# Kernel optimization log

Measured on AMD Instinct MI355X. Metric: run time of the kernel, lower is better.

The kernel has to match this reference:

```python
import jax, jax.numpy as jnp
import numpy as np

B, T, C, NH = 4, 2048, 1024, 16
HS = C // NH


def setup_inputs() -> dict:
    key = jax.random.key(0)
    k1, k2, k3, k4, k5 = jax.random.split(key, 5)
    s = 1.0 / np.sqrt(C)
    return {
        "x": jax.random.normal(k1, (B, T, C), dtype=jnp.float32),
        "Wqkv": jax.random.normal(k2, (3 * C, C), dtype=jnp.float32) * s,
        "bqkv": jax.random.normal(k3, (3 * C,), dtype=jnp.float32) * 0.02,
        "Wproj": jax.random.normal(k4, (C, C), dtype=jnp.float32) * s,
        "bproj": jax.random.normal(k5, (C,), dtype=jnp.float32) * 0.02,
    }


def reference(x, Wqkv, bqkv, Wproj, bproj):
    Bsz, Tlen, Cdim = x.shape
    # qkv projection (torch Linear: x @ W.T + b)
    qkv = x @ Wqkv.T + bqkv                      # [B, T, 3C]
    q, k, v = jnp.split(qkv, 3, axis=-1)
    # [B, NH, T, HS]
    q = q.reshape(Bsz, Tlen, NH, HS).transpose(0, 2, 1, 3)
    k = k.reshape(Bsz, Tlen, NH, HS).transpose(0, 2, 1, 3)
    v = v.reshape(Bsz, Tlen, NH, HS).transpose(0, 2, 1, 3)
    scale = 1.0 / np.sqrt(HS)
    att = jnp.einsum('bhqd,bhkd->bhqk', q, k) * scale
    causal = jnp.triu(jnp.ones((Tlen, Tlen), dtype=bool), k=1)
    att = jnp.where(causal[None, None], -jnp.inf, att)
    att = jax.nn.softmax(att, axis=-1)
    y = jnp.einsum('bhqk,bhkd->bhqd', att, v)    # [B, NH, T, HS]
    y = y.transpose(0, 2, 1, 3).reshape(Bsz, Tlen, Cdim)
    return y @ Wproj.T + bproj
```

## Files before the change

kernel.cpp:

```cpp
#include <hip/hip_runtime.h>
#include <hip/hip_bf16.h>

#define B_   4
#define T_   2048
#define C_   1024
#define NH_  16
#define HS_  64
#define M_   8192
#define N1_  3072
#define BH_  64

typedef __attribute__((ext_vector_type(8))) short short8;
typedef __attribute__((ext_vector_type(4))) short short4v;
typedef __attribute__((ext_vector_type(4))) float f32x4;

#define QSCALE 0.18033688011112042f

__device__ __forceinline__ short f2bf(float f) {
  unsigned u = __float_as_uint(f);
  unsigned r = (u + 0x7fffu + ((u >> 16) & 1u)) >> 16;
  return (short)r;
}
__device__ __forceinline__ unsigned pk_bf16(float a, float b) {
  __hip_bfloat162 h = __float22bfloat162_rn(make_float2(a, b));
  union { __hip_bfloat162 h2; unsigned u; } cv; cv.h2 = h; return cv.u;
}

typedef __attribute__((address_space(1))) unsigned int as1_uint;
typedef __attribute__((address_space(3))) unsigned int as3_uint;
__device__ __forceinline__ void g2l16(const void* g, void* l) {
  __builtin_amdgcn_global_load_lds((as1_uint*)g, (as3_uint*)l, 16, 0, 0);
}

__global__ __launch_bounds__(256) void conv_bf16(
    const float* __restrict__ src, short* __restrict__ dst)
{
  const size_t i = ((size_t)blockIdx.x * 256 + threadIdx.x) * 8;
  const f32x4 a = *(const f32x4*)&src[i];
  const f32x4 b = *(const f32x4*)&src[i + 4];
  short8 o;
  o[0] = f2bf(a[0]); o[1] = f2bf(a[1]); o[2] = f2bf(a[2]); o[3] = f2bf(a[3]);
  o[4] = f2bf(b[0]); o[5] = f2bf(b[1]); o[6] = f2bf(b[2]); o[7] = f2bf(b[3]);
  *(short8*)&dst[i] = o;
}

__global__ __launch_bounds__(256) void qkv_gemm(
    const short* __restrict__ X,
    const short* __restrict__ W,
    const float* __restrict__ bias,
    short* __restrict__ Qo, short* __restrict__ Ko, short* __restrict__ Vt)
{
  __shared__ short As[2][128 * 64];
  __shared__ short Bs[2][128 * 64];
  const int tid = threadIdx.x;
  const int lane = tid & 63;
  const int wid = tid >> 6;
  const int wy = wid >> 1, wx = wid & 1;
  const int lq = lane >> 4, lm = lane & 15;
  const int row0 = blockIdx.x * 128;
  const int col0 = blockIdx.y * 128;

  f32x4 acc[4][4] = {};

  const int ar = tid >> 3;
  const int ac = (tid & 7) << 3;

#pragma unroll
  for (int j = 0; j < 4; ++j) {
    const int r = ar + j * 32;
    g2l16(&X[(size_t)(row0 + r) * C_ + ac], &As[0][r * 64 + ac]);
    g2l16(&W[(size_t)(col0 + r) * C_ + ac], &Bs[0][r * 64 + ac]);
  }
  __syncthreads();

  int cur = 0;
  for (int k0 = 0; k0 < C_; k0 += 64) {
    if (k0 + 64 < C_) {
#pragma unroll
      for (int j = 0; j < 4; ++j) {
        const int r = ar + j * 32;
        g2l16(&X[(size_t)(row0 + r) * C_ + k0 + 64 + ac], &As[cur ^ 1][r * 64 + ac]);
        g2l16(&W[(size_t)(col0 + r) * C_ + k0 + 64 + ac], &Bs[cur ^ 1][r * 64 + ac]);
      }
    }

#pragma unroll
    for (int kk = 0; kk < 2; ++kk) {
      short8 af[4], bfr[4];
#pragma unroll
      for (int mi = 0; mi < 4; ++mi)
        af[mi] = *(const short8*)&As[cur][(wy * 64 + mi * 16 + lm) * 64 + kk * 32 + lq * 8];
#pragma unroll
      for (int ni = 0; ni < 4; ++ni)
        bfr[ni] = *(const short8*)&Bs[cur][(wx * 64 + ni * 16 + lm) * 64 + kk * 32 + lq * 8];
#pragma unroll
      for (int mi = 0; mi < 4; ++mi)
#pragma unroll
        for (int ni = 0; ni < 4; ++ni)
          acc[mi][ni] = __builtin_amdgcn_mfma_f32_16x16x32_bf16(af[mi], bfr[ni], acc[mi][ni], 0, 0, 0);
    }

    __syncthreads();
    cur ^= 1;
  }

#pragma unroll
  for (int ni = 0; ni < 4; ++ni) {
    const int n = col0 + wx * 64 + ni * 16 + lm;
    const float bv = bias[n];
    const int sel = n >> 10;
    const int cc = n & (C_ - 1);
    const int h = cc >> 6, d = cc & 63;
    if (sel == 2) {
#pragma unroll
      for (int mi = 0; mi < 4; ++mi) {
        const int m0 = row0 + wy * 64 + mi * 16 + lq * 4;
        const int b = m0 >> 11, t0 = m0 & (T_ - 1);
        const int bh = b * NH_ + h;
        short4v o;
#pragma unroll
        for (int i = 0; i < 4; ++i) o[i] = f2bf(acc[mi][ni][i] + bv);
        *(short4v*)&Vt[((size_t)bh * HS_ + d) * T_ + t0] = o;
      }
    } else {
      short* dst = (sel == 0) ? Qo : Ko;
      const float qs = (sel == 0) ? QSCALE : 1.0f;
#pragma unroll
      for (int mi = 0; mi < 4; ++mi) {
#pragma unroll
        for (int i = 0; i < 4; ++i) {
          const int m = row0 + wy * 64 + mi * 16 + lq * 4 + i;
          const int b = m >> 11, t = m & (T_ - 1);
          const int bh = b * NH_ + h;
          dst[((size_t)bh * T_ + t) * HS_ + d] = f2bf((acc[mi][ni][i] + bv) * qs);
        }
      }
    }
  }
}

__global__ __launch_bounds__(256) void proj_gemm(
    const short* __restrict__ Y,
    const short* __restrict__ W,
    const float* __restrict__ bias,
    float* __restrict__ Out)
{
  __shared__ short As[2][128 * 64];
  __shared__ short Bs[2][128 * 64];
  const int tid = threadIdx.x;
  const int lane = tid & 63;
  const int wid = tid >> 6;
  const int wy = wid >> 1, wx = wid & 1;
  const int lq = lane >> 4, lm = lane & 15;
  const int row0 = blockIdx.x * 128;
  const int col0 = blockIdx.y * 128;

  f32x4 acc[4][4] = {};

  const int ar = tid >> 3;
  const int ac = (tid & 7) << 3;

#pragma unroll
  for (int j = 0; j < 4; ++j) {
    const int r = ar + j * 32;
    g2l16(&Y[(size_t)(row0 + r) * C_ + ac], &As[0][r * 64 + ac]);
    g2l16(&W[(size_t)(col0 + r) * C_ + ac], &Bs[0][r * 64 + ac]);
  }
  __syncthreads();

  int cur = 0;
  for (int k0 = 0; k0 < C_; k0 += 64) {
    if (k0 + 64 < C_) {
#pragma unroll
      for (int j = 0; j < 4; ++j) {
        const int r = ar + j * 32;
        g2l16(&Y[(size_t)(row0 + r) * C_ + k0 + 64 + ac], &As[cur ^ 1][r * 64 + ac]);
        g2l16(&W[(size_t)(col0 + r) * C_ + k0 + 64 + ac], &Bs[cur ^ 1][r * 64 + ac]);
      }
    }

#pragma unroll
    for (int kk = 0; kk < 2; ++kk) {
      short8 af[4], bfr[4];
#pragma unroll
      for (int mi = 0; mi < 4; ++mi)
        af[mi] = *(const short8*)&As[cur][(wy * 64 + mi * 16 + lm) * 64 + kk * 32 + lq * 8];
#pragma unroll
      for (int ni = 0; ni < 4; ++ni)
        bfr[ni] = *(const short8*)&Bs[cur][(wx * 64 + ni * 16 + lm) * 64 + kk * 32 + lq * 8];
#pragma unroll
      for (int mi = 0; mi < 4; ++mi)
#pragma unroll
        for (int ni = 0; ni < 4; ++ni)
          acc[mi][ni] = __builtin_amdgcn_mfma_f32_16x16x32_bf16(af[mi], bfr[ni], acc[mi][ni], 0, 0, 0);
    }

    __syncthreads();
    cur ^= 1;
  }

#pragma unroll
  for (int ni = 0; ni < 4; ++ni) {
    const int n = col0 + wx * 64 + ni * 16 + lm;
    const float bv = bias[n];
#pragma unroll
    for (int mi = 0; mi < 4; ++mi) {
#pragma unroll
      for (int i = 0; i < 4; ++i) {
        const int m = row0 + wy * 64 + mi * 16 + lq * 4 + i;
        Out[(size_t)m * C_ + n] = acc[mi][ni][i] + bv;
      }
    }
  }
}

#define LDK 72
__global__ __launch_bounds__(512, 4) void attn(
    const short* __restrict__ Qg, const short* __restrict__ Kg,
    const short* __restrict__ Vg, short* __restrict__ Yo)
{
  __shared__ short Ks[64 * LDK];
  __shared__ short Vs[64 * LDK];

  const int tid = threadIdx.x;
  const int lane = tid & 63;
  const int w = tid >> 6;
  const int wq = w & 3;
  const int grp = w >> 2;
  const int lq = lane >> 4, lm = lane & 15;
  const int bh = blockIdx.x;
  const int b = bh >> 4, h = bh & 15;
  const size_t base = (size_t)bh * T_ * HS_;
  const short* __restrict__ Kb = Kg + base;
  const short* __restrict__ Vb = Vg + base;

  const int sr = tid >> 3;
  const int sc = (tid & 7) * 8;

  const int ty = blockIdx.y;
  const int qt = grp ? ty : (15 - ty);
  const int nkt_g = 2 * qt + 2;
  const int nktA = 32 - 2 * ty;

  const int qA = qt * 128 + wq * 16 + lm;
  const int qB = qA + 64;

  const short8 qfA0 = *(const short8*)&Qg[base + (size_t)qA * HS_ + lq * 8];
  const short8 qfA1 = *(const short8*)&Qg[base + (size_t)qA * HS_ + 32 + lq * 8];
  const short8 qfB0 = *(const short8*)&Qg[base + (size_t)qB * HS_ + lq * 8];
  const short8 qfB1 = *(const short8*)&Qg[base + (size_t)qB * HS_ + 32 + lq * 8];

  float lA = 0.0f, lB = 0.0f;
  f32x4 oA[4] = {}, oB[4] = {};

  short8 pk = *(const short8*)&Kb[(size_t)sr * HS_ + sc];
  short8 pv = *(const short8*)&Vb[(size_t)sr * T_ + sc];

#pragma unroll 1
  for (int kt = 0; kt < nktA; ++kt) {
    const int kv0 = kt * 64;

    __syncthreads();
    *(short8*)&Ks[sr * LDK + sc] = pk;
    *(short8*)&Vs[sr * LDK + sc] = pv;
    __syncthreads();

    if (kt + 1 < nktA) {
      pk = *(const short8*)&Kb[(size_t)(kv0 + 64 + sr) * HS_ + sc];
      pv = *(const short8*)&Vb[(size_t)sr * T_ + kv0 + 64 + sc];
    }

    if (kt < nkt_g) {
      const bool doA = (kt <= 2 * qt);

      short8 kf0[4], kf1[4];
#pragma unroll
      for (int ni = 0; ni < 4; ++ni) {
        kf0[ni] = *(const short8*)&Ks[(ni * 16 + lm) * LDK + lq * 8];
        kf1[ni] = *(const short8*)&Ks[(ni * 16 + lm) * LDK + 32 + lq * 8];
      }

      f32x4 svA[4], svB[4];
      if (doA) {
#pragma unroll
        for (int ni = 0; ni < 4; ++ni) {
          f32x4 s = {};
          s = __builtin_amdgcn_mfma_f32_16x16x32_bf16(kf0[ni], qfA0, s, 0, 0, 0);
          svA[ni] = __builtin_amdgcn_mfma_f32_16x16x32_bf16(kf1[ni], qfA1, s, 0, 0, 0);
        }
      }
#pragma unroll
      for (int ni = 0; ni < 4; ++ni) {
        f32x4 s = {};
        s = __builtin_amdgcn_mfma_f32_16x16x32_bf16(kf0[ni], qfB0, s, 0, 0, 0);
        svB[ni] = __builtin_amdgcn_mfma_f32_16x16x32_bf16(kf1[ni], qfB1, s, 0, 0, 0);
      }

      if (kt == 2 * qt) {
#pragma unroll
        for (int ni = 0; ni < 4; ++ni) {
          const int kvb = kv0 + ni * 16 + lq * 4;
#pragma unroll
          for (int i = 0; i < 4; ++i)
            if (kvb + i > qA) svA[ni][i] = -3.0e38f;
        }
      }
      if (kt == 2 * qt + 1) {
#pragma unroll
        for (int ni = 0; ni < 4; ++ni) {
          const int kvb = kv0 + ni * 16 + lq * 4;
#pragma unroll
          for (int i = 0; i < 4; ++i)
            if (kvb + i > qB) svB[ni][i] = -3.0e38f;
        }
      }

      short4v p4A[4], p4B[4];
      if (doA) {
#pragma unroll
        for (int ni = 0; ni < 4; ++ni)
#pragma unroll
          for (int i = 0; i < 4; ++i)
            svA[ni][i] = __builtin_amdgcn_exp2f(svA[ni][i]);
        lA += ((svA[0][0] + svA[0][1]) + (svA[0][2] + svA[0][3]))
            + ((svA[1][0] + svA[1][1]) + (svA[1][2] + svA[1][3]))
            + ((svA[2][0] + svA[2][1]) + (svA[2][2] + svA[2][3]))
            + ((svA[3][0] + svA[3][1]) + (svA[3][2] + svA[3][3]));
#pragma unroll
        for (int ni = 0; ni < 4; ++ni) {
          union { short4v s4; unsigned u[2]; } pk2;
          pk2.u[0] = pk_bf16(svA[ni][0], svA[ni][1]);
          pk2.u[1] = pk_bf16(svA[ni][2], svA[ni][3]);
          p4A[ni] = pk2.s4;
        }
      }
#pragma unroll
      for (int ni = 0; ni < 4; ++ni)
#pragma unroll
        for (int i = 0; i < 4; ++i)
          svB[ni][i] = __builtin_amdgcn_exp2f(svB[ni][i]);
      lB += ((svB[0][0] + svB[0][1]) + (svB[0][2] + svB[0][3]))
          + ((svB[1][0] + svB[1][1]) + (svB[1][2] + svB[1][3]))
          + ((svB[2][0] + svB[2][1]) + (svB[2][2] + svB[2][3]))
          + ((svB[3][0] + svB[3][1]) + (svB[3][2] + svB[3][3]));
#pragma unroll
      for (int ni = 0; ni < 4; ++ni) {
        union { short4v s4; unsigned u[2]; } pk2;
        pk2.u[0] = pk_bf16(svB[ni][0], svB[ni][1]);
        pk2.u[1] = pk_bf16(svB[ni][2], svB[ni][3]);
        p4B[ni] = pk2.s4;
      }

      if (doA) {
#pragma unroll
        for (int di = 0; di < 4; ++di) {
#pragma unroll
          for (int ni = 0; ni < 4; ++ni) {
            const short4v vfr = *(const short4v*)&Vs[(di * 16 + lm) * LDK + ni * 16 + lq * 4];
            oA[di] = __builtin_amdgcn_mfma_f32_16x16x16bf16_1k(vfr, p4A[ni], oA[di], 0, 0, 0);
            oB[di] = __builtin_amdgcn_mfma_f32_16x16x16bf16_1k(vfr, p4B[ni], oB[di], 0, 0, 0);
          }
        }
      } else {
#pragma unroll
        for (int di = 0; di < 4; ++di) {
#pragma unroll
          for (int ni = 0; ni < 4; ++ni) {
            const short4v vfr = *(const short4v*)&Vs[(di * 16 + lm) * LDK + ni * 16 + lq * 4];
            oB[di] = __builtin_amdgcn_mfma_f32_16x16x16bf16_1k(vfr, p4B[ni], oB[di], 0, 0, 0);
          }
        }
      }
    }
  }

  lA += __shfl_xor(lA, 16);
  lA += __shfl_xor(lA, 32);
  lB += __shfl_xor(lB, 16);
  lB += __shfl_xor(lB, 32);
  const float rlA = 1.0f / lA;
  const float rlB = 1.0f / lB;
  const size_t rowA = ((size_t)(b * T_ + qA)) * C_ + h * HS_;
  const size_t rowB = ((size_t)(b * T_ + qB)) * C_ + h * HS_;
#pragma unroll
  for (int di = 0; di < 4; ++di) {
    union { short4v s4; unsigned u[2]; } pk2;
    pk2.u[0] = pk_bf16(oA[di][0] * rlA, oA[di][1] * rlA);
    pk2.u[1] = pk_bf16(oA[di][2] * rlA, oA[di][3] * rlA);
    *(short4v*)&Yo[rowA + di * 16 + lq * 4] = pk2.s4;
    pk2.u[0] = pk_bf16(oB[di][0] * rlB, oB[di][1] * rlB);
    pk2.u[1] = pk_bf16(oB[di][2] * rlB, oB[di][3] * rlB);
    *(short4v*)&Yo[rowB + di * 16 + lq * 4] = pk2.s4;
  }
}

extern "C" void kernel_launch(void* const* d_in, const int* in_sizes, int n_in,
                              void* d_out, int out_size, void* d_ws, size_t ws_size,
                              hipStream_t stream) {
  (void)in_sizes; (void)n_in; (void)out_size;
  const float* x     = (const float*)d_in[0];
  const float* Wqkv  = (const float*)d_in[1];
  const float* bqkv  = (const float*)d_in[2];
  const float* Wproj = (const float*)d_in[3];
  const float* bproj = (const float*)d_in[4];
  float* out = (float*)d_out;

  const size_t nWq = (size_t)N1_ * C_;
  const size_t nWp = (size_t)C_ * C_;
  const size_t nFull = (size_t)M_ * C_;
  const size_t nB = (size_t)T_ * C_;

  dim3 blk(256);
  const size_t need_batched = (nWq + nWp + 4 * nFull) * sizeof(short);

  if (ws_size >= need_batched) {
    short* Wq_bf = (short*)d_ws;
    short* Wp_bf = Wq_bf + nWq;
    short* S0    = Wp_bf + nWp;
    short* Qw    = S0 + nFull;
    short* Kw    = Qw + nFull;
    short* Vw    = Kw + nFull;

    conv_bf16<<<dim3((int)(nWq / 2048)), blk, 0, stream>>>(Wqkv, Wq_bf);
    conv_bf16<<<dim3((int)(nWp / 2048)), blk, 0, stream>>>(Wproj, Wp_bf);
    conv_bf16<<<dim3((int)(nFull / 2048)), blk, 0, stream>>>(x, S0);
    qkv_gemm<<<dim3(M_ / 128, N1_ / 128), blk, 0, stream>>>(S0, Wq_bf, bqkv, Qw, Kw, Vw);
    attn<<<dim3(BH_, 8), dim3(512), 0, stream>>>(Qw, Kw, Vw, S0);
    proj_gemm<<<dim3(M_ / 128, C_ / 128), blk, 0, stream>>>(S0, Wp_bf, bproj, out);
  } else {
    short* Wq_bf = (short*)d_ws;
    short* Wp_bf = Wq_bf + nWq;
    short* S0    = Wp_bf + nWp;
    short* Qw    = S0 + nB;
    short* Kw    = Qw + nB;
    short* Vw    = Kw + nB;

    conv_bf16<<<dim3((int)(nWq / 2048)), blk, 0, stream>>>(Wqkv, Wq_bf);
    conv_bf16<<<dim3((int)(nWp / 2048)), blk, 0, stream>>>(Wproj, Wp_bf);
    for (int b = 0; b < B_; ++b) {
      const float* xb = x   + (size_t)b * nB;
      float*       ob = out + (size_t)b * nB;
      conv_bf16<<<dim3((int)(nB / 2048)), blk, 0, stream>>>(xb, S0);
      qkv_gemm<<<dim3(T_ / 128, N1_ / 128), blk, 0, stream>>>(S0, Wq_bf, bqkv, Qw, Kw, Vw);
      attn<<<dim3(NH_, 8), dim3(512), 0, stream>>>(Qw, Kw, Vw, S0);
      proj_gemm<<<dim3(T_ / 128, C_ / 128), blk, 0, stream>>>(S0, Wp_bf, bproj, ob);
    }
  }
}
```

Baseline: 258.2 us.

## Triple-buffer GEMM mainloop with swizzled LDS and explicit vmcnt waits

Both GEMM kernels move from a double-buffered K=64 tile loop to a three-stage ring of K=32 tiles. Loads are issued two stages ahead, and each step waits with an explicit s_waitcnt vmcnt plus a raw s_barrier instead of __syncthreads. An XOR swizzle on the LDS column offset is meant to reduce bank conflicts on the fragment reads. The aim is to hide global-to-LDS latency better and cut LDS conflicts. The cost is more barriers per unit of K and a dependence on hand-counted vmcnt values being correct.

```diff
diff --git a/kernel.cpp b/kernel.cpp
--- a/kernel.cpp
+++ b/kernel.cpp
@@ -44,65 +44,73 @@
   *(short8*)&dst[i] = o;
 }
 
+#define NT_ 32
+
+#define GEMM_PRELUDE() \
+  const int tid = threadIdx.x; \
+  const int lane = tid & 63; \
+  const int wid = tid >> 6; \
+  const int wy = wid >> 1, wx = wid & 1; \
+  const int lq = lane >> 4, lm = lane & 15; \
+  const int row0 = blockIdx.x * 128; \
+  const int col0 = blockIdx.y * 128; \
+  f32x4 acc[4][4] = {}; \
+  const int s0 = tid, s1 = tid + 256;             \
+  const int r0 = s0 >> 2, r1 = s1 >> 2;           \
+  const int c0s = ((s0 & 3) ^ ((r0 >> 1) & 3)) * 8;   \
+  const int c1s = ((s1 & 3) ^ ((r1 >> 1) & 3)) * 8; \
+  const int rsw = (lq ^ ((lm >> 1) & 3)) * 8;
+
+#define GEMM_STAGE(PA, PB, k0, bi) do { \
+    g2l16(&PA[(size_t)(row0 + r0) * C_ + (k0) + c0s], &As[bi][s0 * 8]); \
+    g2l16(&PA[(size_t)(row0 + r1) * C_ + (k0) + c1s], &As[bi][s1 * 8]); \
+    g2l16(&PB[(size_t)(col0 + r0) * C_ + (k0) + c0s], &Bs[bi][s0 * 8]); \
+    g2l16(&PB[(size_t)(col0 + r1) * C_ + (k0) + c1s], &Bs[bi][s1 * 8]); \
+  } while (0)
+
+#define GEMM_MAINLOOP(PA, PB) \
+  GEMM_STAGE(PA, PB, 0, 0); \
+  GEMM_STAGE(PA, PB, 32, 1); \
+  int cur = 0; \
+  for (int t = 0; t < NT_; ++t) { \
+    if (t < NT_ - 1) { asm volatile("s_waitcnt vmcnt(4)" ::: "memory"); } \
+    else             { asm volatile("s_waitcnt vmcnt(0)" ::: "memory"); } \
+    __builtin_amdgcn_sched_barrier(0); \
+    __builtin_amdgcn_s_barrier(); \
+    __builtin_amdgcn_sched_barrier(0); \
+    { \
+      const short* Ab = &As[cur][0]; \
+      const short* Bb = &Bs[cur][0]; \
+      short8 af[4], bfr[4]; \
+      _Pragma("unroll") \
+      for (int mi = 0; mi < 4; ++mi) \
+        af[mi] = *(const short8*)&Ab[(wy * 64 + mi * 16 + lm) * 32 + rsw]; \
+      _Pragma("unroll") \
+      for (int ni = 0; ni < 4; ++ni) \
+        bfr[ni] = *(const short8*)&Bb[(wx * 64 + ni * 16 + lm) * 32 + rsw]; \
+      _Pragma("unroll") \
+      for (int mi = 0; mi < 4; ++mi) \
+        _Pragma("unroll") \
+        for (int ni = 0; ni < 4; ++ni) \
+          acc[mi][ni] = __builtin_amdgcn_mfma_f32_16x16x32_bf16(af[mi], bfr[ni], acc[mi][ni], 0, 0, 0); \
+    } \
+    if (t + 2 < NT_) { \
+      const int bi2 = (cur + 2) - ((cur + 2) >= 3 ? 3 : 0); \
+      GEMM_STAGE(PA, PB, (t + 2) * 32, bi2); \
+    } \
+    cur = (cur + 1) - ((cur + 1) >= 3 ? 3 : 0); \
+  }
+
 __global__ __launch_bounds__(256) void qkv_gemm(
     const short* __restrict__ X,
     const short* __restrict__ W,
     const float* __restrict__ bias,
     short* __restrict__ Qo, short* __restrict__ Ko, short* __restrict__ Vt)
 {
-  __shared__ short As[2][128 * 64];
-  __shared__ short Bs[2][128 * 64];
-  const int tid = threadIdx.x;
-  const int lane = tid & 63;
-  const int wid = tid >> 6;
-  const int wy = wid >> 1, wx = wid & 1;
-  const int lq = lane >> 4, lm = lane & 15;
-  const int row0 = blockIdx.x * 128;
-  const int col0 = blockIdx.y * 128;
-
-  f32x4 acc[4][4] = {};
-
-  const int ar = tid >> 3;
-  const int ac = (tid & 7) << 3;
-
-#pragma unroll
-  for (int j = 0; j < 4; ++j) {
-    const int r = ar + j * 32;
-    g2l16(&X[(size_t)(row0 + r) * C_ + ac], &As[0][r * 64 + ac]);
-    g2l16(&W[(size_t)(col0 + r) * C_ + ac], &Bs[0][r * 64 + ac]);
-  }
-  __syncthreads();
-
-  int cur = 0;
-  for (int k0 = 0; k0 < C_; k0 += 64) {
-    if (k0 + 64 < C_) {
-#pragma unroll
-      for (int j = 0; j < 4; ++j) {
-        const int r = ar + j * 32;
-        g2l16(&X[(size_t)(row0 + r) * C_ + k0 + 64 + ac], &As[cur ^ 1][r * 64 + ac]);
-        g2l16(&W[(size_t)(col0 + r) * C_ + k0 + 64 + ac], &Bs[cur ^ 1][r * 64 + ac]);
-      }
-    }
-
-#pragma unroll
-    for (int kk = 0; kk < 2; ++kk) {
-      short8 af[4], bfr[4];
-#pragma unroll
-      for (int mi = 0; mi < 4; ++mi)
-        af[mi] = *(const short8*)&As[cur][(wy * 64 + mi * 16 + lm) * 64 + kk * 32 + lq * 8];
-#pragma unroll
-      for (int ni = 0; ni < 4; ++ni)
-        bfr[ni] = *(const short8*)&Bs[cur][(wx * 64 + ni * 16 + lm) * 64 + kk * 32 + lq * 8];
-#pragma unroll
-      for (int mi = 0; mi < 4; ++mi)
-#pragma unroll
-        for (int ni = 0; ni < 4; ++ni)
-          acc[mi][ni] = __builtin_amdgcn_mfma_f32_16x16x32_bf16(af[mi], bfr[ni], acc[mi][ni], 0, 0, 0);
-    }
-
-    __syncthreads();
-    cur ^= 1;
-  }
+  __shared__ short As[3][128 * 32];
+  __shared__ short Bs[3][128 * 32];
+  GEMM_PRELUDE();
+  GEMM_MAINLOOP(X, W);
 
 #pragma unroll
   for (int ni = 0; ni < 4; ++ni) {
@@ -145,59 +153,10 @@
     const float* __restrict__ bias,
     float* __restrict__ Out)
 {
-  __shared__ short As[2][128 * 64];
-  __shared__ short Bs[2][128 * 64];
-  const int tid = threadIdx.x;
-  const int lane = tid & 63;
-  const int wid = tid >> 6;
-  const int wy = wid >> 1, wx = wid & 1;
-  const int lq = lane >> 4, lm = lane & 15;
-  const int row0 = blockIdx.x * 128;
-  const int col0 = blockIdx.y * 128;
-
-  f32x4 acc[4][4] = {};
-
-  const int ar = tid >> 3;
-  const int ac = (tid & 7) << 3;
-
-#pragma unroll
-  for (int j = 0; j < 4; ++j) {
-    const int r = ar + j * 32;
-    g2l16(&Y[(size_t)(row0 + r) * C_ + ac], &As[0][r * 64 + ac]);
-    g2l16(&W[(size_t)(col0 + r) * C_ + ac], &Bs[0][r * 64 + ac]);
-  }
-  __syncthreads();
-
-  int cur = 0;
-  for (int k0 = 0; k0 < C_; k0 += 64) {
-    if (k0 + 64 < C_) {
-#pragma unroll
-      for (int j = 0; j < 4; ++j) {
-        const int r = ar + j * 32;
-        g2l16(&Y[(size_t)(row0 + r) * C_ + k0 + 64 + ac], &As[cur ^ 1][r * 64 + ac]);
-        g2l16(&W[(size_t)(col0 + r) * C_ + k0 + 64 + ac], &Bs[cur ^ 1][r * 64 + ac]);
-      }
-    }
-
-#pragma unroll
-    for (int kk = 0; kk < 2; ++kk) {
-      short8 af[4], bfr[4];
-#pragma unroll
-      for (int mi = 0; mi < 4; ++mi)
-        af[mi] = *(const short8*)&As[cur][(wy * 64 + mi * 16 + lm) * 64 + kk * 32 + lq * 8];
-#pragma unroll
-      for (int ni = 0; ni < 4; ++ni)
-        bfr[ni] = *(const short8*)&Bs[cur][(wx * 64 + ni * 16 + lm) * 64 + kk * 32 + lq * 8];
-#pragma unroll
-      for (int mi = 0; mi < 4; ++mi)
-#pragma unroll
-        for (int ni = 0; ni < 4; ++ni)
-          acc[mi][ni] = __builtin_amdgcn_mfma_f32_16x16x32_bf16(af[mi], bfr[ni], acc[mi][ni], 0, 0, 0);
-    }
-
-    __syncthreads();
-    cur ^= 1;
-  }
+  __shared__ short As[3][128 * 32];
+  __shared__ short Bs[3][128 * 32];
+  GEMM_PRELUDE();
+  GEMM_MAINLOOP(Y, W);
 
 #pragma unroll
   for (int ni = 0; ni < 4; ++ni) {
```

Measured after the change: 248.2 us. -3.9%, faster.
